# Optimization experiments

Hardware: AMD Instinct MI355X
Metric: run time of the kernel (lower is better)

The kernel has to match this reference:

```python
import jax, jax.numpy as jnp
import numpy as np


def _conv3(x, w):
    # 3x3 conv, stride 1, padding 1 (SAME), NCHW/OIHW
    return jax.lax.conv_general_dilated(
        x, w, window_strides=(1, 1), padding=((1, 1), (1, 1)),
        dimension_numbers=("NCHW", "OIHW", "NCHW"))


def setup_inputs() -> dict:
    key = jax.random.key(0)
    ks = jax.random.split(key, 10)
    B, C, H, W = 16, 64, 128, 128
    NL = 4
    inp = {
        "x0": jax.random.normal(ks[0], (B, C, H, W), dtype=jnp.float32),
        "spa_mask": jax.random.uniform(ks[1], (B, 1, H, W), dtype=jnp.float32),
        # uniform noise in (0,1) for gumbel; bounded away from 0 like the torch retry loop
        "gumbels": jax.random.uniform(ks[2], (1, C, NL, 2), dtype=jnp.float32,
                                      minval=1e-6, maxval=1.0 - 1e-6),
        "ch_mask_param": jax.random.uniform(ks[3], (1, C, NL, 2), dtype=jnp.float32),
        "w0": jax.random.normal(ks[4], (C, C, 3, 3), dtype=jnp.float32) * 0.05,
        "w1": jax.random.normal(ks[5], (C, C, 3, 3), dtype=jnp.float32) * 0.05,
        "w2": jax.random.normal(ks[6], (C, C, 3, 3), dtype=jnp.float32) * 0.05,
        "w3": jax.random.normal(ks[7], (C, C, 3, 3), dtype=jnp.float32) * 0.05,
        "wc": jax.random.normal(ks[8], (C, C * NL, 1, 1), dtype=jnp.float32) * 0.05,
        "bc": jax.random.normal(ks[9], (C,), dtype=jnp.float32) * 0.05,
    }
    return inp


def reference(x0, spa_mask, gumbels, ch_mask_param, w0, w1, w2, w3, wc, bc):
    tau = 1.0
    g = -jnp.log(-jnp.log(gumbels))
    ch_mask = jax.nn.softmax((ch_mask_param + g) / tau, axis=3)  # (1,C,NL,2)
    ws = [w0, w1, w2, w3]
    outs = []
    fea = x0
    for i in range(4):
        m_d = ch_mask[:, :, i, 0][:, :, None, None]  # dense-path channel gate (1,C,1,1)
        m_s = ch_mask[:, :, i, 1][:, :, None, None]  # sparse-path channel gate
        if i == 0:
            fea = _conv3(fea, ws[0])
            fea = fea * m_s * spa_mask + fea * m_d
        else:
            fea_d = _conv3(fea * m_d, ws[i])
            fea_s = _conv3(fea * m_s, ws[i])
            fea = (fea_d * m_s * spa_mask + fea_d * m_d
                   + fea_s * m_s * spa_mask + fea_s * m_d * spa_mask)
        fea = jax.nn.relu(fea)
        outs.append(fea)
    cat = jnp.concatenate(outs, axis=1)  # (B, 4C, H, W)
    out = jnp.einsum("oc,bchw->bohw", wc[:, :, 0, 0], cat) + bc[None, :, None, None]
    return (out, ch_mask)
```

## Files before the change

### kernel.cpp

```cpp
#include <hip/hip_runtime.h>
#include <math.h>

#define B_ 16
#define C_ 64
#define H_ 128
#define W_ 128
#define HW_ (H_*W_)
#define OUT_ELEMS 16777216

#define CHM_B    0
#define PWA_B    2048
#define AH_B     34816
#define FEA_B(s) (550912u + (size_t)(s)*33554432u)

#define A_S0   0
#define A_S(s) (36864 + ((s)-1)*73728)

typedef __attribute__((ext_vector_type(4))) short  v4s;
typedef __attribute__((ext_vector_type(8))) short  v8s;
typedef __attribute__((ext_vector_type(4))) float  v4f;

__device__ __forceinline__ ushort f2bf(float f) {
    unsigned u = __builtin_bit_cast(unsigned, f);
    unsigned r = u + 0x7FFFu + ((u >> 16) & 1u);
    return (ushort)(r >> 16);
}

__global__ __launch_bounds__(64) void mask_kernel(
    const float* __restrict__ gum, const float* __restrict__ par,
    float* __restrict__ chm, float* __restrict__ out_tail)
{
    int c = threadIdx.x;
    #pragma unroll
    for (int i = 0; i < 4; ++i) {
        int base = (c*4 + i)*2;
        float g0 = -logf(-logf(gum[base]));
        float g1 = -logf(-logf(gum[base+1]));
        float a0 = par[base] + g0, a1 = par[base+1] + g1;
        float mx = fmaxf(a0, a1);
        float e0 = expf(a0 - mx), e1 = expf(a1 - mx);
        float inv = 1.0f / (e0 + e1);
        float m0 = e0*inv, m1 = e1*inv;
        chm[base] = m0; chm[base+1] = m1;
        out_tail[base] = m0; out_tail[base+1] = m1;
    }
}

__global__ __launch_bounds__(256) void prep_kernel(
    const float* __restrict__ w0, const float* __restrict__ w1,
    const float* __restrict__ w2, const float* __restrict__ w3,
    const float* __restrict__ wc, const float* __restrict__ chm,
    ushort* __restrict__ AH, ushort* __restrict__ pwA)
{
    int idx = blockIdx.x*256 + threadIdx.x;
    if (idx < 36864) {
        int blk = idx >> 11;
        int r3  = idx & 2047;
        int oc = r3 >> 5, icl = r3 & 31;
        int cc = blk / 9, t = blk - 9*cc;
        int ic = cc*32 + icl;
        AH[idx] = f2bf(w0[(oc*64 + ic)*9 + t]);
    } else if (idx < 258048) {
        int j = idx - 36864;
        int s = 1 + j / 73728;
        int r = j % 73728;
        int blk = r >> 12;
        int r3  = r & 4095;
        int ocM = r3 >> 5, icl = r3 & 31;
        int cc = blk / 9, t = blk - 9*cc;
        int ic = cc*32 + icl;
        int oc = ocM >> 1, set = ocM & 1;
        const float* wsrc = (s == 1) ? w1 : (s == 2 ? w2 : w3);
        AH[idx] = f2bf(wsrc[(oc*64 + ic)*9 + t] * chm[(ic*4 + s)*2 + set]);
    } else {
        int r = idx - 258048;
        pwA[r] = f2bf(wc[r]);
    }
}

template<int NSETS, bool INF32>
__global__ __launch_bounds__(256, 2) void conv_bf16(
    const void* __restrict__ inv, const ushort* __restrict__ A,
    const float* __restrict__ chm, const float* __restrict__ spa,
    ushort* __restrict__ feaOut, int stage)
{
    constexpr int MOC = 64*NSETS;
    constexpr int MT  = MOC/32;
    __shared__ __align__(16) ushort sB[3*130*36];

    const int tid  = threadIdx.x;
    const int lane = tid & 63, wave = tid >> 6;
    const int wrow = wave >> 1, wcol = wave & 1;
    const int q = lane >> 4, ln16 = lane & 15;
    const int wk = (blockIdx.x & 7)*256 + (blockIdx.x >> 3);
    const int h = wk & 127, b = wk >> 7;

    v4f acc[MT][4];
    #pragma unroll
    for (int m = 0; m < MT; ++m)
        #pragma unroll
        for (int n = 0; n < 4; ++n) acc[m][n] = (v4f){0.f, 0.f, 0.f, 0.f};

    int aRow[MT];
    #pragma unroll
    for (int m = 0; m < MT; ++m)
        aRow[m] = (wrow*(MOC/2) + m*16 + ln16)*32 + q*8;

    v8s stg[6];
    v4f stgF[12];
    v8s af[4][MT];

    auto issue = [&](int ic0) {
        #pragma unroll
        for (int it = 0; it < 6; ++it) {
            int i  = it*256 + tid;
            int ry = i >> 9;
            int r  = i & 511;
            int ic = r >> 4, wv = r & 15;
            int gh = h - 1 + ry;
            if constexpr (INF32) {
                v4f a0 = (v4f){0.f,0.f,0.f,0.f}, a1 = a0;
                if ((unsigned)gh < 128u) {
                    const float* s = (const float*)inv +
                        ((size_t)((b*C_ + ic0 + ic)*H_ + gh)*W_ + wv*8);
                    a0 = *(const v4f*)(const void*)s;
                    a1 = *(const v4f*)(const void*)(s + 4);
                }
                stgF[it*2] = a0; stgF[it*2+1] = a1;
            } else {
                v8s v = (v8s){0,0,0,0,0,0,0,0};
                if ((unsigned)gh < 128u)
                    v = *(const v8s*)(const void*)((const ushort*)inv +
                        ((size_t)((b*C_ + ic0 + ic)*H_ + gh)*W_ + wv*8));
                stg[it] = v;
            }
        }
    };
    auto scatter = [&]() {
        #pragma unroll
        for (int it = 0; it < 6; ++it) {
            int i  = it*256 + tid;
            int ry = i >> 9;
            int r  = i & 511;
            int ic = r >> 4, wv = r & 15;
            int colBase = ry*130 + wv*8 + 1;
            ushort vals[8];
            if constexpr (INF32) {
                #pragma unroll
                for (int j = 0; j < 4; ++j) {
                    vals[j]   = f2bf(stgF[it*2][j]);
                    vals[4+j] = f2bf(stgF[it*2+1][j]);
                }
            } else {
                #pragma unroll
                for (int j = 0; j < 8; ++j) vals[j] = (ushort)stg[it][j];
            }
            #pragma unroll
            for (int j = 0; j < 8; ++j) {
                int colIdx = colBase + j;
                int s3 = (colIdx >> 3) & 7;
                sB[colIdx*36 + (ic ^ (s3 << 2))] = vals[j];
            }
        }
    };
    auto prolog = [&](const ushort* Ab) {
        #pragma unroll
        for (int tp = 0; tp < 3; ++tp)
            #pragma unroll
            for (int m = 0; m < MT; ++m)
                af[tp][m] = *(const v8s*)(const void*)(Ab + tp*MOC*32 + aRow[m]);
    };
    auto compute = [&](const ushort* Ab) {
        #pragma unroll
        for (int t = 0; t < 9; ++t) {
            if (t < 6) {
                #pragma unroll
                for (int m = 0; m < MT; ++m)
                    af[(t+3)&3][m] = *(const v8s*)(const void*)(Ab + (t+3)*MOC*32 + aRow[m]);
            }
            const int ky = t/3, kx = t - 3*(t/3);
            #pragma unroll
            for (int nt = 0; nt < 4; ++nt) {
                int colIdx = ky*130 + wcol*64 + nt*16 + ln16 + kx;
                int s3 = (colIdx >> 3) & 7;
                int base = colIdx*36 + ((q ^ (s3 >> 1)) << 3);
                int lo = base + ((s3 & 1) << 2);
                int hi = base + (((s3 & 1) ^ 1) << 2);
                v4s va = *(const v4s*)(const void*)(sB + lo);
                v4s vb = *(const v4s*)(const void*)(sB + hi);
                v8s bf = __builtin_shufflevector(va, vb, 0, 1, 2, 3, 4, 5, 6, 7);
                #pragma unroll
                for (int m = 0; m < MT; ++m)
                    acc[m][nt] = __builtin_amdgcn_mfma_f32_16x16x32_bf16(af[t&3][m], bf, acc[m][nt], 0, 0, 0);
            }
        }
    };

    issue(0);
    prolog(A);
    if (tid < 216) {
        int colSel = tid / 36;
        int icz    = tid - colSel*36;
        int ry     = colSel >> 1;
        int colIdx = ry*130 + ((colSel & 1) ? 129 : 0);
        sB[colIdx*36 + icz] = 0;
    }
    scatter();
    issue(32);
    __syncthreads();
    compute(A);
    prolog(A + 9*MOC*32);
    __syncthreads();
    scatter();
    __syncthreads();
    compute(A + 9*MOC*32);

    const float* spaRow = &spa[b*HW_ + h*W_];
    #pragma unroll
    for (int nt = 0; nt < 4; ++nt) {
        int px = wcol*64 + nt*16 + ln16;
        float sp = spaRow[px];
        #pragma unroll
        for (int m = 0; m < MT; ++m) {
            if constexpr (NSETS == 2) {
                #pragma unroll
                for (int rp = 0; rp < 2; ++rp) {
                    int oc = wrow*32 + m*8 + q*2 + rp;
                    float md = chm[(oc*4 + stage)*2 + 0];
                    float ms = chm[(oc*4 + stage)*2 + 1];
                    float f = acc[m][nt][2*rp]*(ms*sp + md)
                            + acc[m][nt][2*rp+1]*((ms + md)*sp);
                    feaOut[((size_t)(b*C_ + oc)*H_ + h)*W_ + px] = f2bf(fmaxf(f, 0.f));
                }
            } else {
                #pragma unroll
                for (int r = 0; r < 4; ++r) {
                    int oc = wrow*32 + m*16 + q*4 + r;
                    float md = chm[(oc*4 + stage)*2 + 0];
                    float ms = chm[(oc*4 + stage)*2 + 1];
                    float f = acc[m][nt][r]*(ms*sp + md);
                    feaOut[((size_t)(b*C_ + oc)*H_ + h)*W_ + px] = f2bf(fmaxf(f, 0.f));
                }
            }
        }
    }
}

__global__ __launch_bounds__(256, 2) void pw_final(
    const ushort* __restrict__ fea, const ushort* __restrict__ pwA,
    const float* __restrict__ bc, float* __restrict__ out)
{
    __shared__ __align__(16) ushort sF[64*260];

    const int tid  = threadIdx.x;
    const int lane = tid & 63, wave = tid >> 6;
    const int wrow = wave >> 1, wcol = wave & 1;
    const int q = lane >> 4, ln16 = lane & 15;
    const int half = blockIdx.x & 1;
    const int h = (blockIdx.x >> 1) & 127;
    const int b = blockIdx.x >> 8;
    const int px0 = half*64;

    {
        v8s stg[8];
        #pragma unroll
        for (int it = 0; it < 8; ++it) {
            int i  = it*256 + tid;
            int s  = i >> 9;
            int r  = i & 511;
            int ic = r >> 3, pxv = r & 7;
            stg[it] = *(const v8s*)(const void*)(
                fea + (size_t)s*OUT_ELEMS + ((size_t)(b*C_ + ic)*H_ + h)*W_ + px0 + pxv*8);
        }
        #pragma unroll
        for (int it = 0; it < 8; ++it) {
            int i  = it*256 + tid;
            int s  = i >> 9;
            int r  = i & 511;
            int ic = r >> 3, pxv = r & 7;
            int kS = (s*64 + ic) ^ ((pxv & 3) << 3);
            ushort* dst = &sF[(pxv*8)*260 + kS];
            #pragma unroll
            for (int j = 0; j < 8; ++j) dst[j*260] = (ushort)stg[it][j];
        }
    }
    __syncthreads();

    v4f acc[2][2];
    #pragma unroll
    for (int m = 0; m < 2; ++m)
        #pragma unroll
        for (int n = 0; n < 2; ++n) acc[m][n] = (v4f){0.f, 0.f, 0.f, 0.f};

    #pragma unroll
    for (int ks = 0; ks < 8; ++ks) {
        v8s a[2];
        #pragma unroll
        for (int m = 0; m < 2; ++m)
            a[m] = *(const v8s*)(const void*)(pwA + (wrow*32 + m*16 + ln16)*256 + ks*32 + q*8);
        #pragma unroll
        for (int n = 0; n < 2; ++n) {
            int px = wcol*32 + n*16 + ln16;
            int swz = (px >> 3) & 3;
            v4s va = *(const v4s*)(const void*)(sF + px*260 + ks*32 + ((q ^ swz) << 3));
            v4s vb = *(const v4s*)(const void*)(sF + px*260 + ks*32 + ((q ^ swz) << 3) + 4);
            v8s bf = __builtin_shufflevector(va, vb, 0, 1, 2, 3, 4, 5, 6, 7);
            #pragma unroll
            for (int m = 0; m < 2; ++m)
                acc[m][n] = __builtin_amdgcn_mfma_f32_16x16x32_bf16(a[m], bf, acc[m][n], 0, 0, 0);
        }
    }

    #pragma unroll
    for (int n = 0; n < 2; ++n) {
        int px = px0 + wcol*32 + n*16 + ln16;
        #pragma unroll
        for (int m = 0; m < 2; ++m)
            #pragma unroll
            for (int r = 0; r < 4; ++r) {
                int o = wrow*32 + m*16 + q*4 + r;
                out[((size_t)(b*C_ + o)*H_ + h)*W_ + px] = acc[m][n][r] + bc[o];
            }
    }
}

extern "C" void kernel_launch(void* const* d_in, const int* in_sizes, int n_in,
                              void* d_out, int out_size, void* d_ws, size_t ws_size,
                              hipStream_t stream)
{
    const float* x0  = (const float*)d_in[0];
    const float* spa = (const float*)d_in[1];
    const float* gum = (const float*)d_in[2];
    const float* par = (const float*)d_in[3];
    const float* w0  = (const float*)d_in[4];
    const float* w1  = (const float*)d_in[5];
    const float* w2  = (const float*)d_in[6];
    const float* w3  = (const float*)d_in[7];
    const float* wc  = (const float*)d_in[8];
    const float* bc  = (const float*)d_in[9];
    float* out = (float*)d_out;
    char*  ws  = (char*)d_ws;

    float*  chm = (float*)(ws + CHM_B);
    ushort* pwA = (ushort*)(ws + PWA_B);
    ushort* AH  = (ushort*)(ws + AH_B);
    ushort* fea0 = (ushort*)(ws + FEA_B(0));
    ushort* fea1 = (ushort*)(ws + FEA_B(1));
    ushort* fea2 = (ushort*)(ws + FEA_B(2));
    ushort* fea3 = (ushort*)(ws + FEA_B(3));

    mask_kernel<<<1, 64, 0, stream>>>(gum, par, chm, out + OUT_ELEMS);
    prep_kernel<<<1072, 256, 0, stream>>>(w0, w1, w2, w3, wc, chm, AH, pwA);

    conv_bf16<1, true ><<<2048, 256, 0, stream>>>(x0,   AH + A_S0,  chm, spa, fea0, 0);
    conv_bf16<2, false><<<2048, 256, 0, stream>>>(fea0, AH + A_S(1), chm, spa, fea1, 1);
    conv_bf16<2, false><<<2048, 256, 0, stream>>>(fea1, AH + A_S(2), chm, spa, fea2, 2);
    conv_bf16<2, false><<<2048, 256, 0, stream>>>(fea2, AH + A_S(3), chm, spa, fea3, 3);

    pw_final<<<4096, 256, 0, stream>>>(fea0, pwA, bc, out);
}
```

Baseline: 417.7 us.

## Load both input-channel halves into LDS up front and run one fused MFMA loop

The conv kernel now stages both 32-channel halves of the input rows into two separate LDS buffers before a single barrier, then runs one continuous 18-step MFMA loop across both halves. This removes two barriers and the mid-kernel scatter phase, and lets the weight-fragment prefetch run straight across the half boundary. In exchange it doubles the LDS footprint and the staging registers (stg/stgF arrays grow to 12/24 vectors), which may reduce occupancy below the 2 blocks per CU the launch bounds request, or cause register spills. It also no longer overlaps the second half's global loads with the first half's compute.

```diff
diff --git a/kernel.cpp b/kernel.cpp
--- a/kernel.cpp
+++ b/kernel.cpp
@@ -15,6 +15,8 @@
 
 #define A_S0   0
 #define A_S(s) (36864 + ((s)-1)*73728)
+
+#define SUBT 14040
 
 typedef __attribute__((ext_vector_type(4))) short  v4s;
 typedef __attribute__((ext_vector_type(8))) short  v8s;
@@ -86,7 +88,7 @@
 {
     constexpr int MOC = 64*NSETS;
     constexpr int MT  = MOC/32;
-    __shared__ __align__(16) ushort sB[3*130*36];
+    __shared__ __align__(16) ushort sB[2*SUBT];
 
     const int tid  = threadIdx.x;
     const int lane = tid & 63, wave = tid >> 6;
@@ -106,11 +108,12 @@
     for (int m = 0; m < MT; ++m)
         aRow[m] = (wrow*(MOC/2) + m*16 + ln16)*32 + q*8;
 
-    v8s stg[6];
-    v4f stgF[12];
+    v8s stg[12];
+    v4f stgF[24];
     v8s af[4][MT];
 
-    auto issue = [&](int ic0) {
+    auto issue = [&](int c) {
+        const int ic0 = c*32;
         #pragma unroll
         for (int it = 0; it < 6; ++it) {
             int i  = it*256 + tid;
@@ -126,17 +129,18 @@
                     a0 = *(const v4f*)(const void*)s;
                     a1 = *(const v4f*)(const void*)(s + 4);
                 }
-                stgF[it*2] = a0; stgF[it*2+1] = a1;
+                stgF[(c*6+it)*2] = a0; stgF[(c*6+it)*2+1] = a1;
             } else {
                 v8s v = (v8s){0,0,0,0,0,0,0,0};
                 if ((unsigned)gh < 128u)
                     v = *(const v8s*)(const void*)((const ushort*)inv +
                         ((size_t)((b*C_ + ic0 + ic)*H_ + gh)*W_ + wv*8));
-                stg[it] = v;
+                stg[c*6+it] = v;
             }
         }
     };
-    auto scatter = [&]() {
+    auto scatter = [&](int c) {
+        ushort* sBc = sB + c*SUBT;
         #pragma unroll
         for (int it = 0; it < 6; ++it) {
             int i  = it*256 + tid;
@@ -148,37 +152,39 @@
             if constexpr (INF32) {
                 #pragma unroll
                 for (int j = 0; j < 4; ++j) {
-                    vals[j]   = f2bf(stgF[it*2][j]);
-                    vals[4+j] = f2bf(stgF[it*2+1][j]);
+                    vals[j]   = f2bf(stgF[(c*6+it)*2][j]);
+                    vals[4+j] = f2bf(stgF[(c*6+it)*2+1][j]);
                 }
             } else {
                 #pragma unroll
-                for (int j = 0; j < 8; ++j) vals[j] = (ushort)stg[it][j];
+                for (int j = 0; j < 8; ++j) vals[j] = (ushort)stg[c*6+it][j];
             }
             #pragma unroll
             for (int j = 0; j < 8; ++j) {
                 int colIdx = colBase + j;
                 int s3 = (colIdx >> 3) & 7;
-                sB[colIdx*36 + (ic ^ (s3 << 2))] = vals[j];
+                sBc[colIdx*36 + (ic ^ (s3 << 2))] = vals[j];
             }
         }
     };
-    auto prolog = [&](const ushort* Ab) {
+    auto prolog = [&]() {
         #pragma unroll
         for (int tp = 0; tp < 3; ++tp)
             #pragma unroll
             for (int m = 0; m < MT; ++m)
-                af[tp][m] = *(const v8s*)(const void*)(Ab + tp*MOC*32 + aRow[m]);
+                af[tp][m] = *(const v8s*)(const void*)(A + tp*MOC*32 + aRow[m]);
     };
-    auto compute = [&](const ushort* Ab) {
-        #pragma unroll
-        for (int t = 0; t < 9; ++t) {
-            if (t < 6) {
+    auto computeAll = [&]() {
+        #pragma unroll
+        for (int tt = 0; tt < 18; ++tt) {
+            if (tt < 15) {
                 #pragma unroll
                 for (int m = 0; m < MT; ++m)
-                    af[(t+3)&3][m] = *(const v8s*)(const void*)(Ab + (t+3)*MOC*32 + aRow[m]);
-            }
+                    af[(tt+3)&3][m] = *(const v8s*)(const void*)(A + (tt+3)*MOC*32 + aRow[m]);
+            }
+            const int c  = tt/9, t = tt - 9*c;
             const int ky = t/3, kx = t - 3*(t/3);
+            const ushort* sBc = sB + c*SUBT;
             #pragma unroll
             for (int nt = 0; nt < 4; ++nt) {
                 int colIdx = ky*130 + wcol*64 + nt*16 + ln16 + kx;
@@ -186,34 +192,31 @@
                 int base = colIdx*36 + ((q ^ (s3 >> 1)) << 3);
                 int lo = base + ((s3 & 1) << 2);
                 int hi = base + (((s3 & 1) ^ 1) << 2);
-                v4s va = *(const v4s*)(const void*)(sB + lo);
-                v4s vb = *(const v4s*)(const void*)(sB + hi);
+                v4s va = *(const v4s*)(const void*)(sBc + lo);
+                v4s vb = *(const v4s*)(const void*)(sBc + hi);
                 v8s bf = __builtin_shufflevector(va, vb, 0, 1, 2, 3, 4, 5, 6, 7);
                 #pragma unroll
                 for (int m = 0; m < MT; ++m)
-                    acc[m][nt] = __builtin_amdgcn_mfma_f32_16x16x32_bf16(af[t&3][m], bf, acc[m][nt], 0, 0, 0);
+                    acc[m][nt] = __builtin_amdgcn_mfma_f32_16x16x32_bf16(af[tt&3][m], bf, acc[m][nt], 0, 0, 0);
             }
         }
     };
 
     issue(0);
-    prolog(A);
+    issue(1);
+    prolog();
     if (tid < 216) {
         int colSel = tid / 36;
         int icz    = tid - colSel*36;
         int ry     = colSel >> 1;
         int colIdx = ry*130 + ((colSel & 1) ? 129 : 0);
         sB[colIdx*36 + icz] = 0;
-    }
-    scatter();
-    issue(32);
+        sB[SUBT + colIdx*36 + icz] = 0;
+    }
+    scatter(0);
+    scatter(1);
     __syncthreads();
-    compute(A);
-    prolog(A + 9*MOC*32);
-    __syncthreads();
-    scatter();
-    __syncthreads();
-    compute(A + 9*MOC*32);
+    computeAll();
 
     const float* spaRow = &spa[b*HW_ + h*W_];
     #pragma unroll
```

After: 388.5 us. 7.0% less time.
